# Kernel optimization log

Measured on AMD Instinct MI355X. Metric: run time of the kernel, lower is better.

The kernel has to match this reference:

```python
import jax, jax.numpy as jnp
import numpy as np
from jax import lax

NUM_HOP = 2      # opt.num_hop
POOL_HOP = 1     # Encoder(..., num_hop=1) in gnn_pools
K_POOL = 1024    # int(pooling_ratio * num_patches) = 0.5 * 2048
TH = 0.0         # opt.nonzero_th
T = 0.07         # NCE temperature
NEG_FILL = -10.0


def l2norm(x):
    # Normalize(power=2): x / (sum(x^2, dim=1, keepdim)^(1/2))
    return x / jnp.sqrt(jnp.sum(x * x, axis=1, keepdims=True))


def tagconv(A, h, W, b, k):
    # DGL TAGConv: concat_{i=0..k} (D^-1/2 A D^-1/2)^i h, then linear
    deg = jnp.sum(A, axis=1)
    dinv = lax.rsqrt(jnp.maximum(deg, 1e-12))
    An = A * dinv[:, None] * dinv[None, :]   # [N,N] normalized adjacency
    feats = [h]
    for _ in range(k):
        h = An @ h
        feats.append(h)
    return jnp.concatenate(feats, axis=1) @ W + b


def nce_pair(f_t, f_s):
    # calc_gnn NCE: positives = diag(f_t . f_s); negatives = full gram with diag masked to -10
    n = f_t.shape[0]
    eye = jnp.eye(n, dtype=bool)
    pos = jnp.sum(f_t * f_s, axis=1, keepdims=True)          # [N,1]
    neg_s = jnp.where(eye, NEG_FILL, f_t @ f_s.T)            # [N,N]
    neg_t = jnp.where(eye, NEG_FILL, f_s @ f_t.T)
    out_s = jnp.concatenate([pos, neg_s], axis=1) / T
    out_t = jnp.concatenate([pos, neg_t], axis=1) / T
    # CrossEntropy with label 0 == -log_softmax(out)[:, 0], mean over rows
    loss_s = -jnp.mean(jax.nn.log_softmax(out_s, axis=1)[:, 0])
    loss_t = -jnp.mean(jax.nn.log_softmax(out_t, axis=1)[:, 0])
    return loss_s + loss_t


def setup_inputs() -> dict:
    key = jax.random.key(0)
    ks = jax.random.split(key, 8)
    N, C, D = 2048, 512, 128
    g = 0.02  # init_gain ('normal' init)
    return {
        "fs": jax.random.normal(ks[0], (N, C), jnp.float32),
        "ft": jax.random.normal(ks[1], (N, C), jnp.float32),
        "W_embed": g * jax.random.normal(ks[2], (C, D), jnp.float32),
        "b_embed": jnp.zeros((D,), jnp.float32),
        "W_gnn": g * jax.random.normal(ks[3], ((NUM_HOP + 1) * D, D), jnp.float32),
        "b_gnn": jnp.zeros((D,), jnp.float32),
        "W_pool": g * jax.random.normal(ks[4], (D, 1), jnp.float32),
        "b_pool": jnp.zeros((1,), jnp.float32),
        "W_gnnp": g * jax.random.normal(ks[5], ((POOL_HOP + 1) * D, D), jnp.float32),
        "b_gnnp": jnp.zeros((D,), jnp.float32),
    }


def reference(fs, ft, W_embed, b_embed, W_gnn, b_gnn, W_pool, b_pool, W_gnnp, b_gnnp):
    # Embed: linear + l2 norm
    f_es = l2norm(fs @ W_embed + b_embed)   # student [N, nc]
    f_et = l2norm(ft @ W_embed + b_embed)   # teacher [N, nc]

    # nonzero_graph on detached teacher features; same adjacency reused for student
    ft_d = lax.stop_gradient(f_et)
    n = f_et.shape[0]
    eye = jnp.eye(n, dtype=bool)
    A = (ft_d @ ft_d.T > TH).astype(f_et.dtype)
    A = jnp.where(eye, 1.0, A)  # dgl.add_self_loop

    # TAGConv encoder + l2norm; teacher branch detached
    f_gt = lax.stop_gradient(l2norm(tagconv(A, f_et, W_gnn, b_gnn, NUM_HOP)))
    f_gs = l2norm(tagconv(A, f_es, W_gnn, b_gnn, NUM_HOP))
    loss_g = nce_pair(f_gt, f_gs)

    # Pool / top_k_graph
    scores = jax.nn.sigmoid((f_gt @ W_pool + b_pool)[:, 0])   # [N]
    vals, idx = lax.top_k(scores, K_POOL)
    new_ht = f_gt[idx] * vals[:, None]
    new_hs = f_gs[idx] * vals[:, None]
    un = (A > 0).astype(A.dtype)
    un2 = ((un @ un) > 0).astype(A.dtype)        # 2-hop boolean adjacency
    sub = un2[idx][:, idx]                       # [k,k]
    deg = jnp.sum(sub, axis=1)
    g_pool = sub / deg[None, :]                  # replicates torch broadcast in norm_g(g/degrees)

    # pooled-stage Encoder (TAGConv k=1) on the pooled graph structure (with self loops)
    k = K_POOL
    eye_k = jnp.eye(k, dtype=bool)
    Ap = (g_pool > 0).astype(A.dtype)
    Ap = jnp.where(eye_k, 1.0, Ap)
    f_pt = lax.stop_gradient(l2norm(tagconv(Ap, new_ht, W_gnnp, b_gnnp, POOL_HOP)))
    f_ps = l2norm(tagconv(Ap, new_hs, W_gnnp, b_gnnp, POOL_HOP))
    loss_pool = nce_pair(f_pt, f_ps)

    return loss_g + loss_pool
```

## Files before the change

kernel.cpp:

```cpp
#include <hip/hip_runtime.h>


#define TINV (1.0f / 0.07f)

using short8 = __attribute__((ext_vector_type(8))) short;
using f32x4  = __attribute__((ext_vector_type(4))) float;

__device__ __forceinline__ unsigned short f2bf(float f) {
    unsigned u = __float_as_uint(f);
    u += 0x7fff + ((u >> 16) & 1);
    return (unsigned short)(u >> 16);
}

template<bool BT>
__device__ __forceinline__ void mm_tile(const float* __restrict__ A, int lda,
                                        const float* __restrict__ B, int ldb,
                                        int i0, int j0, int k0, int k1,
                                        float (&acc)[4][4],
                                        float (&As)[16][68], float (&Bs)[16][68])
{
    const int tid = threadIdx.x;
    const int tx = tid & 15;
    const int ty = tid >> 4;
    const int lr = tid >> 2;
    const int lc = (tid & 3) * 4;
    for (int k = k0; k < k1; k += 16) {
        float4 av = *(const float4*)(A + (size_t)(i0 + lr) * lda + (k + lc));
        As[lc + 0][lr] = av.x; As[lc + 1][lr] = av.y;
        As[lc + 2][lr] = av.z; As[lc + 3][lr] = av.w;
        if (BT) {
            float4 bv = *(const float4*)(B + (size_t)(j0 + lr) * ldb + (k + lc));
            Bs[lc + 0][lr] = bv.x; Bs[lc + 1][lr] = bv.y;
            Bs[lc + 2][lr] = bv.z; Bs[lc + 3][lr] = bv.w;
        } else {
            const int n = tid & 63;
            const int kb = tid >> 6;
#pragma unroll
            for (int it = 0; it < 4; ++it)
                Bs[kb * 4 + it][n] = B[(size_t)(k + kb * 4 + it) * ldb + (j0 + n)];
        }
        __syncthreads();
#pragma unroll
        for (int kk = 0; kk < 16; ++kk) {
            float a[4], b[4];
#pragma unroll
            for (int u = 0; u < 4; ++u) a[u] = As[kk][ty * 4 + u];
#pragma unroll
            for (int v = 0; v < 4; ++v) b[v] = Bs[kk][tx * 4 + v];
#pragma unroll
            for (int u = 0; u < 4; ++u)
#pragma unroll
                for (int v = 0; v < 4; ++v)
                    acc[u][v] = fmaf(a[u], b[v], acc[u][v]);
        }
        __syncthreads();
    }
}

__launch_bounds__(256)
__global__ void k_setup_embed(const float* __restrict__ fs, const float* __restrict__ ft,
                              const float* __restrict__ W, float* __restrict__ part,
                              size_t zstr, int* __restrict__ zwords, int zcount,
                              float* __restrict__ out,
                              const float* __restrict__ Wg, const float* __restrict__ Wp,
                              unsigned short* __restrict__ Wtall)
{
    __shared__ float As[16][68];
    __shared__ float Bs[16][68];
    const int b = blockIdx.x;
    const int tid = threadIdx.x;
    if (b < 512) {
        const int z = b & 3;
        const int by = (b >> 2) & 63;
        const int bx = b >> 8;
        const float* A = (by < 32) ? ft : fs;
        const int i0 = (by & 31) * 64;
        const int j0 = bx * 64;
        float acc[4][4] = {};
        mm_tile<false>(A, 512, W, 128, i0, j0, z * 128, z * 128 + 128, acc, As, Bs);
        const int tx = tid & 15, ty = tid >> 4;
        float* dst = part + (size_t)z * zstr;
#pragma unroll
        for (int u = 0; u < 4; ++u) {
            const size_t ri = (size_t)(by * 64 + ty * 4 + u) * 128 + j0 + tx * 4;
            float4 vv;
            vv.x = acc[u][0]; vv.y = acc[u][1]; vv.z = acc[u][2]; vv.w = acc[u][3];
            *(float4*)(dst + ri) = vv;
        }
    } else if (b < 561) {
        const int i = (b - 512) * 256 + tid;
        if (i < zcount) zwords[i] = 0;
        if (b == 512 && tid == 0) out[0] = 0.0f;
    } else {
        const int e0 = (b - 561) * 2048 + tid;
#pragma unroll
        for (int it = 0; it < 8; ++it) {
            const int e = e0 + it * 256;
            const int c = e >> 14;
            const int rem = e & 16383;
            const int n = rem >> 7, k = rem & 127;
            const float* src = (c < 3) ? (Wg + (size_t)c * 16384)
                                       : (Wp + (size_t)(c - 3) * 16384);
            Wtall[e] = f2bf(src[(size_t)k * 128 + n]);
        }
    }
}

__launch_bounds__(256)
__global__ void k_gram_fused(const float* __restrict__ f_e,
                             unsigned short* __restrict__ A01,
                             unsigned long long* __restrict__ bits,
                             int* __restrict__ deg)
{
    __shared__ float As[16][68];
    __shared__ float Bs[16][68];
    __shared__ unsigned char nib[64][16];
    __shared__ unsigned char nibT[64][16];
    __shared__ unsigned long long chk[64];
    __shared__ unsigned long long chkT[64];
    const int b = blockIdx.x;
    int by = (int)((sqrtf(8.0f * b + 1.0f) - 1.0f) * 0.5f);
    while ((by + 1) * (by + 2) / 2 <= b) ++by;
    while (by * (by + 1) / 2 > b) --by;
    const int bx = b - by * (by + 1) / 2;
    const int i0 = by * 64, j0 = bx * 64;
    float acc[4][4] = {};
    mm_tile<true>(f_e, 128, f_e, 128, i0, j0, 0, 128, acc, As, Bs);
    const int tid = threadIdx.x;
    const int tx = tid & 15, ty = tid >> 4;
    unsigned pb = 0;
#pragma unroll
    for (int u = 0; u < 4; ++u)
#pragma unroll
        for (int v = 0; v < 4; ++v) {
            bool pred = (acc[u][v] > 0.0f) || (i0 + ty * 4 + u == j0 + tx * 4 + v);
            pb |= (unsigned)pred << (u * 4 + v);
        }
#pragma unroll
    for (int u = 0; u < 4; ++u) nib[ty * 4 + u][tx] = (pb >> (4 * u)) & 15;
#pragma unroll
    for (int v = 0; v < 4; ++v) {
        unsigned nt = 0;
#pragma unroll
        for (int u = 0; u < 4; ++u) nt |= ((pb >> (u * 4 + v)) & 1u) << u;
        nibT[tx * 4 + v][ty] = nt;
    }
    __syncthreads();
    if (tid < 64) {
        unsigned long long c = 0;
#pragma unroll
        for (int t = 0; t < 16; ++t) c |= (unsigned long long)nib[tid][t] << (4 * t);
        chk[tid] = c;
        bits[(size_t)(i0 + tid) * 32 + (j0 >> 6)] = c;
        atomicAdd(&deg[i0 + tid], __popcll(c));
    } else if (tid < 128 && bx != by) {
        const int r = tid - 64;
        unsigned long long c = 0;
#pragma unroll
        for (int t = 0; t < 16; ++t) c |= (unsigned long long)nibT[r][t] << (4 * t);
        chkT[r] = c;
        bits[(size_t)(j0 + r) * 32 + (i0 >> 6)] = c;
        atomicAdd(&deg[j0 + r], __popcll(c));
    }
    __syncthreads();
#pragma unroll
    for (int it = 0; it < 4; ++it) {
        const int row = it * 16 + (tid >> 4);
        const int c0 = (tid & 15) * 4;
        unsigned short o[4];
#pragma unroll
        for (int c = 0; c < 4; ++c)
            o[c] = ((chk[row] >> (c0 + c)) & 1) ? (unsigned short)0x3F80 : (unsigned short)0;
        *(ulonglong1*)&A01[(size_t)(i0 + row) * 2048 + j0 + c0] = *(ulonglong1*)o;
        if (bx != by) {
            unsigned short o2[4];
#pragma unroll
            for (int c = 0; c < 4; ++c)
                o2[c] = ((chkT[row] >> (c0 + c)) & 1) ? (unsigned short)0x3F80 : (unsigned short)0;
            *(ulonglong1*)&A01[(size_t)(j0 + row) * 2048 + i0 + c0] = *(ulonglong1*)o2;
        }
    }
}

__launch_bounds__(256)
__global__ void mm_bf16(const unsigned short* __restrict__ A, int lda, size_t aZ,
                        const unsigned short* __restrict__ B, int ldb, size_t bZ,
                        float* __restrict__ C, int ldc, size_t cZ,
                        int Kc, int kZ)
{
    __shared__ unsigned short As[64][40];
    __shared__ unsigned short Bs[128][40];
    const int tid = threadIdx.x;
    const int bz = blockIdx.z;
    const int i0 = blockIdx.y * 64;
    const int j0 = blockIdx.x * 128;
    const int k0 = bz * kZ;
    const unsigned short* Ab = A + (size_t)bz * aZ;
    const unsigned short* Bb = B + (size_t)bz * bZ;
    float* Cb = C + (size_t)bz * cZ;
    const int w = tid >> 6;
    const int lane = tid & 63;
    const int m = lane & 15;
    const int q = lane >> 4;
    f32x4 acc[8];
#pragma unroll
    for (int t = 0; t < 8; ++t)
#pragma unroll
        for (int r = 0; r < 4; ++r) acc[t][r] = 0.0f;

    const int ar = tid >> 2;
    const int ac = (tid & 3) * 8;
    for (int ks = 0; ks < Kc; ks += 32) {
        const int k = k0 + ks;
        *(ulonglong2*)&As[ar][ac] =
            *(const ulonglong2*)(Ab + (size_t)(i0 + ar) * lda + k + ac);
        *(ulonglong2*)&Bs[ar][ac] =
            *(const ulonglong2*)(Bb + (size_t)(j0 + ar) * ldb + k + ac);
        *(ulonglong2*)&Bs[ar + 64][ac] =
            *(const ulonglong2*)(Bb + (size_t)(j0 + ar + 64) * ldb + k + ac);
        __syncthreads();
        short8 a = *(const short8*)&As[w * 16 + m][q * 8];
#pragma unroll
        for (int nt = 0; nt < 8; ++nt) {
            short8 b = *(const short8*)&Bs[nt * 16 + m][q * 8];
            acc[nt] = __builtin_amdgcn_mfma_f32_16x16x32_bf16(a, b, acc[nt], 0, 0, 0);
        }
        __syncthreads();
    }
#pragma unroll
    for (int nt = 0; nt < 8; ++nt) {
        const int col = j0 + nt * 16 + m;
#pragma unroll
        for (int r = 0; r < 4; ++r) {
            const int row = i0 + w * 16 + q * 4 + r;
            Cb[(size_t)row * ldc + col] = acc[nt][r];
        }
    }
}

__global__ void reduce_hop(const float* __restrict__ part, int nz, size_t zstr,
                           int M, const float* __restrict__ dinv,
                           unsigned short* __restrict__ hb,
                           unsigned short* __restrict__ xt)
{
    __shared__ float T[32][33];
    const int tid = threadIdx.x;
    const int iloc = tid >> 3, nq = (tid & 7) * 4;
    const int n = blockIdx.x * 32 + nq;
    const int i = blockIdx.y * 32 + iloc;
    float4 s = *(const float4*)(part + (size_t)i * 256 + n);
    for (int z = 1; z < nz; ++z) {
        float4 t = *(const float4*)(part + (size_t)z * zstr + (size_t)i * 256 + n);
        s.x += t.x; s.y += t.y; s.z += t.z; s.w += t.w;
    }
    const float d = dinv[i];
    unsigned short o[4] = { f2bf(s.x * d), f2bf(s.y * d), f2bf(s.z * d), f2bf(s.w * d) };
    const int hrow = (n >= 128 ? M : 0) + i;
    *(ulonglong1*)(hb + (size_t)hrow * 128 + (n & 127)) = *(ulonglong1*)o;
    if (xt) {
        const float d2 = d * d;
        T[nq + 0][iloc] = s.x * d2; T[nq + 1][iloc] = s.y * d2;
        T[nq + 2][iloc] = s.z * d2; T[nq + 3][iloc] = s.w * d2;
        __syncthreads();
        const int nloc = tid >> 3, ic = (tid & 7) * 4;
        unsigned short o2[4];
#pragma unroll
        for (int c = 0; c < 4; ++c) o2[c] = f2bf(T[nloc][ic + c]);
        *(ulonglong1*)(xt + (size_t)(blockIdx.x * 32 + nloc) * M + blockIdx.y * 32 + ic) =
            *(ulonglong1*)o2;
    }
}

__global__ void combine_norm(const float* __restrict__ part, int nz, size_t zstr,
                             const float* __restrict__ bias,
                             float* __restrict__ f32out,
                             unsigned short* __restrict__ bf16out,
                             const float* __restrict__ Wp, const float* __restrict__ bp,
                             float* __restrict__ scores)
{
    const int row = blockIdx.x;
    const int tid = threadIdx.x;
    float v = bias[tid];
    for (int z = 0; z < nz; ++z) v += part[(size_t)z * zstr + (size_t)row * 128 + tid];
    __shared__ float red[128];
    red[tid] = v * v;
    __syncthreads();
    for (int s = 64; s > 0; s >>= 1) {
        if (tid < s) red[tid] += red[tid + s];
        __syncthreads();
    }
    const float o = v * (1.0f / sqrtf(red[0]));
    if (f32out)  f32out[(size_t)row * 128 + tid] = o;
    if (bf16out) bf16out[(size_t)row * 128 + tid] = f2bf(o);
    if (scores && row < 2048) {
        __syncthreads();
        red[tid] = o * Wp[tid];
        __syncthreads();
        for (int s = 64; s > 0; s >>= 1) {
            if (tid < s) red[tid] += red[tid + s];
            __syncthreads();
        }
        if (tid == 0) scores[row] = 1.0f / (1.0f + expf(-(red[0] + bp[0])));
    }
}

__global__ void make_xt(const float* __restrict__ f_e, const int* __restrict__ deg,
                        unsigned short* __restrict__ xt, float* __restrict__ dinv)
{
    __shared__ float T[32][33];
    const int b = blockIdx.x;
    const int bx = b & 7, by = b >> 3;
    const int tid = threadIdx.x;
    const int iloc = tid >> 3, nq = (tid & 7) * 4;
    const int n0 = bx * 32;
    const int i = by * 32 + iloc;
    const int srow = (n0 >= 128 ? 2048 : 0) + i;
    float4 f = *(const float4*)(f_e + (size_t)srow * 128 + ((n0 + nq) & 127));
    const float d = 1.0f / sqrtf((float)deg[i]);
    if (bx == 0 && (tid & 7) == 0) dinv[i] = d;
    T[nq + 0][iloc] = f.x * d; T[nq + 1][iloc] = f.y * d;
    T[nq + 2][iloc] = f.z * d; T[nq + 3][iloc] = f.w * d;
    __syncthreads();
    const int nloc = tid >> 3, ic = (tid & 7) * 4;
    unsigned short o[4];
#pragma unroll
    for (int c = 0; c < 4; ++c) o[c] = f2bf(T[nloc][ic + c]);
    *(ulonglong1*)(xt + (size_t)(n0 + nloc) * 2048 + by * 32 + ic) = *(ulonglong1*)o;
}

__launch_bounds__(256)
__global__ void k_nce_topk(const unsigned short* __restrict__ A,
                           const unsigned short* __restrict__ B,
                           float* __restrict__ rowsum, float* __restrict__ colsum,
                           float* __restrict__ pos, int gramBlocks, int bw,
                           const float* __restrict__ scores,
                           float* __restrict__ vals, int* __restrict__ idx)
{
    __shared__ unsigned short As[64][40];
    __shared__ unsigned short Bs[128][40];
    __shared__ float colbuf[4][128];
    __shared__ unsigned sv[2048];
    __shared__ int hist[256];
    __shared__ int shp, shr, sh_base, sh_out, wsum[5];
    const int tid = threadIdx.x;
    const int b = blockIdx.x;
    if (b < gramBlocks) {
        const int bx = b % bw, by = b / bw;
        const int i0 = by * 64;
        const int j0 = bx * 128;
        const int w = tid >> 6;
        const int lane = tid & 63;
        const int m = lane & 15;
        const int q = lane >> 4;
        f32x4 acc[8];
#pragma unroll
        for (int t = 0; t < 8; ++t)
#pragma unroll
            for (int r = 0; r < 4; ++r) acc[t][r] = 0.0f;
        const int ar = tid >> 2;
        const int ac = (tid & 3) * 8;
        for (int k = 0; k < 128; k += 32) {
            *(ulonglong2*)&As[ar][ac] =
                *(const ulonglong2*)(A + (size_t)(i0 + ar) * 128 + k + ac);
            *(ulonglong2*)&Bs[ar][ac] =
                *(const ulonglong2*)(B + (size_t)(j0 + ar) * 128 + k + ac);
            *(ulonglong2*)&Bs[ar + 64][ac] =
                *(const ulonglong2*)(B + (size_t)(j0 + ar + 64) * 128 + k + ac);
            __syncthreads();
            short8 a = *(const short8*)&As[w * 16 + m][q * 8];
#pragma unroll
            for (int nt = 0; nt < 8; ++nt) {
                short8 bb = *(const short8*)&Bs[nt * 16 + m][q * 8];
                acc[nt] = __builtin_amdgcn_mfma_f32_16x16x32_bf16(a, bb, acc[nt], 0, 0, 0);
            }
            __syncthreads();
        }
        float rpart[4] = {0.0f, 0.0f, 0.0f, 0.0f};
        float cpart[8];
#pragma unroll
        for (int nt = 0; nt < 8; ++nt) {
            const int col = j0 + nt * 16 + m;
            float cs = 0.0f;
#pragma unroll
            for (int r = 0; r < 4; ++r) {
                const int row = i0 + w * 16 + q * 4 + r;
                float g = acc[nt][r];
                float e = __expf(g * TINV);
                if (row == col) { pos[row] = g; e = 0.0f; }
                rpart[r] += e;
                cs += e;
            }
            cpart[nt] = cs;
        }
#pragma unroll
        for (int r = 0; r < 4; ++r) {
            float v = rpart[r];
            v += __shfl_xor(v, 1); v += __shfl_xor(v, 2);
            v += __shfl_xor(v, 4); v += __shfl_xor(v, 8);
            if (m == 0) atomicAdd(&rowsum[i0 + w * 16 + q * 4 + r], v);
        }
#pragma unroll
        for (int nt = 0; nt < 8; ++nt) {
            float v = cpart[nt];
            v += __shfl_xor(v, 16); v += __shfl_xor(v, 32);
            if (q == 0) colbuf[w][nt * 16 + m] = v;
        }
        __syncthreads();
        if (tid < 128) {
            float v = colbuf[0][tid] + colbuf[1][tid] + colbuf[2][tid] + colbuf[3][tid];
            atomicAdd(&colsum[j0 + tid], v);
        }
    } else {
        for (int e = tid; e < 2048; e += 256) sv[e] = __float_as_uint(scores[e]);
        if (tid == 0) { shp = 0; shr = 1024; sh_base = 0; sh_out = 0; }
        __syncthreads();
        for (int byte = 3; byte >= 0; --byte) {
            hist[tid] = 0;
            __syncthreads();
            const unsigned pref = (unsigned)shp;
            const unsigned pmask = (byte == 3) ? 0u : (0xFFFFFFFFu << ((byte + 1) * 8));
            for (int e = tid; e < 2048; e += 256) {
                unsigned u = sv[e];
                if ((u & pmask) == (pref & pmask))
                    atomicAdd(&hist[(u >> (byte * 8)) & 255], 1);
            }
            __syncthreads();
            if (tid == 0) {
                int rem = shr, bs = 255;
                for (; bs > 0; --bs) {
                    if (hist[bs] >= rem) break;
                    rem -= hist[bs];
                }
                shp = (int)(pref | ((unsigned)bs << (byte * 8)));
                shr = rem;
            }
            __syncthreads();
        }
        const unsigned t = (unsigned)shp;
        const int remain = shr;
        const int lane = tid & 63, wave = tid >> 6;
        for (int pass = 0; pass < 8; ++pass) {
            const int e = pass * 256 + tid;
            const unsigned u = sv[e];
            const bool eq = (u == t);
            unsigned long long mk = __ballot(eq);
            int wpre = __popcll(mk & ((1ull << lane) - 1ull));
            if (lane == 0) wsum[wave] = __popcll(mk);
            __syncthreads();
            if (tid == 0) {
                int a = sh_base;
                for (int ww = 0; ww < 4; ++ww) { int c = wsum[ww]; wsum[ww] = a; a += c; }
                sh_base = a;
            }
            __syncthreads();
            const int rank = eq ? (wsum[wave] + wpre) : 0x7fffffff;
            if ((u > t) || (eq && rank < remain)) {
                int slot = atomicAdd(&sh_out, 1);
                idx[slot] = e;
                vals[slot] = __uint_as_float(u);
            }
            __syncthreads();
        }
    }
}

__global__ void k_final_ap(const float* __restrict__ rs, const float* __restrict__ cs,
                           const float* __restrict__ pos, float* __restrict__ out,
                           const unsigned long long* __restrict__ bits,
                           const int* __restrict__ idx,
                           unsigned short* __restrict__ Ap, int* __restrict__ degp)
{
    __shared__ unsigned long long pb[32][33];
    __shared__ unsigned long long qb[32][33];
    __shared__ float red[256];
    const int b = blockIdx.x;
    const int tid = threadIdx.x;
    if (b < 1024) {
        const int tp = (b >> 5) * 32;
        const int tq = (b & 31) * 32;
        for (int t = tid; t < 1024; t += 256) {
            int r = t >> 5, w = t & 31;
            pb[r][w] = bits[(size_t)idx[tp + r] * 32 + w];
            qb[r][w] = bits[(size_t)idx[tq + r] * 32 + w];
        }
        __syncthreads();
        const int pi = tid >> 3;
        const int qc0 = (tid & 7) * 4;
        unsigned long long a0 = 0, a1 = 0, a2 = 0, a3 = 0;
#pragma unroll
        for (int w = 0; w < 32; ++w) {
            const unsigned long long p = pb[pi][w];
            a0 |= p & qb[qc0 + 0][w];
            a1 |= p & qb[qc0 + 1][w];
            a2 |= p & qb[qc0 + 2][w];
            a3 |= p & qb[qc0 + 3][w];
        }
        unsigned short o[4] = { (unsigned short)(a0 ? 0x3F80 : 0),
                                (unsigned short)(a1 ? 0x3F80 : 0),
                                (unsigned short)(a2 ? 0x3F80 : 0),
                                (unsigned short)(a3 ? 0x3F80 : 0) };
        *(ulonglong1*)&Ap[(size_t)(tp + pi) * 1024 + tq + qc0] = *(ulonglong1*)o;
        int v = (a0 ? 1 : 0) + (a1 ? 1 : 0) + (a2 ? 1 : 0) + (a3 ? 1 : 0);
        v += __shfl_xor(v, 1); v += __shfl_xor(v, 2); v += __shfl_xor(v, 4);
        if ((tid & 7) == 0) atomicAdd(&degp[tp + pi], v);
    } else {
        const int i = (b - 1024) * 256 + tid;
        float p = pos[i] * TINV;
        float ep = __expf(p);
        float t = (logf(rs[i] + ep) - p) + (logf(cs[i] + ep) - p);
        red[tid] = t;
        __syncthreads();
        for (int s = 128; s > 0; s >>= 1) {
            if (tid < s) red[tid] += red[tid + s];
            __syncthreads();
        }
        if (tid == 0) atomicAdd(out, red[0] * (1.0f / 2048.0f));
    }
}

__global__ void nce_final(const float* __restrict__ rs, const float* __restrict__ cs,
                          const float* __restrict__ pos, float invN,
                          float* __restrict__ out)
{
    const int i = blockIdx.x * 256 + threadIdx.x;
    float p = pos[i] * TINV;
    float ep = __expf(p);
    float t = (logf(rs[i] + ep) - p) + (logf(cs[i] + ep) - p);
    __shared__ float red[256];
    red[threadIdx.x] = t;
    __syncthreads();
    for (int s = 128; s > 0; s >>= 1) {
        if (threadIdx.x < s) red[threadIdx.x] += red[threadIdx.x + s];
        __syncthreads();
    }
    if (threadIdx.x == 0) atomicAdd(out, red[0] * invN);
}

__global__ void gather_xt(const float* __restrict__ f_g, const int* __restrict__ idx,
                          const float* __restrict__ vals, const int* __restrict__ degp,
                          unsigned short* __restrict__ new_hb,
                          unsigned short* __restrict__ xtp, float* __restrict__ dinvp)
{
    __shared__ float T[32][33];
    const int b = blockIdx.x;
    const int bx = b & 7, by = b >> 3;
    const int tid = threadIdx.x;
    const int ploc = tid >> 3, nq = (tid & 7) * 4;
    const int n0 = bx * 32;
    const int p = by * 32 + ploc;
    const int s = idx[p];
    const float v = vals[p];
    const float dp = 1.0f / sqrtf((float)degp[p]);
    if (bx == 0 && (tid & 7) == 0) dinvp[p] = dp;
    const int srow = (n0 >= 128 ? 2048 : 0) + s;
    float4 f = *(const float4*)(f_g + (size_t)srow * 128 + ((n0 + nq) & 127));
    f.x *= v; f.y *= v; f.z *= v; f.w *= v;
    unsigned short o[4] = { f2bf(f.x), f2bf(f.y), f2bf(f.z), f2bf(f.w) };
    const int hrow = (n0 >= 128 ? 1024 : 0) + p;
    *(ulonglong1*)(new_hb + (size_t)hrow * 128 + ((n0 + nq) & 127)) = *(ulonglong1*)o;
    T[nq + 0][ploc] = f.x * dp; T[nq + 1][ploc] = f.y * dp;
    T[nq + 2][ploc] = f.z * dp; T[nq + 3][ploc] = f.w * dp;
    __syncthreads();
    const int nloc = tid >> 3, pc = (tid & 7) * 4;
    unsigned short o2[4];
#pragma unroll
    for (int c = 0; c < 4; ++c) o2[c] = f2bf(T[nloc][pc + c]);
    *(ulonglong1*)(xtp + (size_t)(n0 + nloc) * 1024 + by * 32 + pc) = *(ulonglong1*)o2;
}

extern "C" void kernel_launch(void* const* d_in, const int* in_sizes, int n_in,
                              void* d_out, int out_size, void* d_ws, size_t ws_size,
                              hipStream_t stream)
{
    (void)in_sizes; (void)n_in; (void)out_size; (void)ws_size;
    const float* fs      = (const float*)d_in[0];
    const float* ft      = (const float*)d_in[1];
    const float* W_embed = (const float*)d_in[2];
    const float* b_embed = (const float*)d_in[3];
    const float* W_gnn   = (const float*)d_in[4];
    const float* b_gnn   = (const float*)d_in[5];
    const float* W_pool  = (const float*)d_in[6];
    const float* b_pool  = (const float*)d_in[7];
    const float* W_gnnp  = (const float*)d_in[8];
    const float* b_gnnp  = (const float*)d_in[9];
    float* out = (float*)d_out;

    float* ws = (float*)d_ws;
    size_t o = 0;
    auto alloc = [&](size_t n) { float* p = ws + o; o += (n + 3) & ~3ull; return p; };
    float* bigB   = alloc(2048ull * 2048);
    float* f_e    = alloc(4096 * 128);
    float* f_g    = alloc(4096 * 128);
    unsigned short* A01  = (unsigned short*)alloc(2048ull * 2048 / 2);
    unsigned short* febT = (unsigned short*)alloc(3ull * 4096 * 128 / 2);
    unsigned short* Xt1  = (unsigned short*)alloc(256ull * 2048 / 2);
    unsigned short* Xt2  = (unsigned short*)alloc(256ull * 2048 / 2);
    unsigned short* f_gb = (unsigned short*)alloc(4096ull * 128 / 2);
    unsigned short* Wtall= (unsigned short*)alloc(5ull * 16384 / 2);
    unsigned short* Ap01 = (unsigned short*)alloc(1024ull * 1024 / 2);
    unsigned short* nhb  = (unsigned short*)alloc(2ull * 2048 * 128 / 2);
    unsigned short* Xtp  = (unsigned short*)alloc(256ull * 1024 / 2);
    unsigned short* f_pb = (unsigned short*)alloc(2048ull * 128 / 2);
    float* dinv   = alloc(2048);
    float* scores = alloc(2048);
    float* vals   = alloc(1024);
    int*   idxb   = (int*)alloc(1024);
    float* dinvp  = alloc(1024);
    unsigned long long* bits = (unsigned long long*)alloc(2048 * 32 * 2);
    float* nceb = alloc(9216);
    int*   deg  = (int*)alloc(2048);
    int*   degp = (int*)alloc(1024);
    const int kZeroCount = 9216 + 2048 + 1024;

    const size_t FSTR = 4096ull * 128;
    const size_t PSTR = 1024ull * 256;
    unsigned short* feb = febT;
    unsigned short* h1b = febT + FSTR;
    unsigned short* h2b = febT + 2 * FSTR;
    unsigned short* tmpb = nhb + 2048ull * 128;
    unsigned short* Wt  = Wtall;
    unsigned short* WtP = Wtall + 3ull * 16384;
    float* rs  = nceb;
    float* csu = nceb + 2048;
    float* pos = nceb + 4096;
    float* rsp  = nceb + 6144;
    float* csp  = nceb + 7168;
    float* posp = nceb + 8192;

    k_setup_embed<<<601, 256, 0, stream>>>(fs, ft, W_embed, bigB, FSTR,
                                           (int*)nceb, kZeroCount, out, W_gnn, W_gnnp, Wtall);
    combine_norm<<<4096, 128, 0, stream>>>(bigB, 4, FSTR, b_embed, f_e, feb,
                                           nullptr, nullptr, nullptr);
    k_gram_fused<<<528, 256, 0, stream>>>(f_e, A01, bits, deg);
    make_xt<<<512, 256, 0, stream>>>(f_e, deg, Xt1, dinv);
    mm_bf16<<<dim3(2, 32, 4), 256, 0, stream>>>(A01, 2048, 0, Xt1, 2048, 0,
                                                bigB, 256, FSTR, 512, 512);
    reduce_hop<<<dim3(8, 64), 256, 0, stream>>>(bigB, 4, FSTR, 2048, dinv, h1b, Xt2);
    mm_bf16<<<dim3(2, 32, 4), 256, 0, stream>>>(A01, 2048, 0, Xt2, 2048, 0,
                                                bigB, 256, FSTR, 512, 512);
    reduce_hop<<<dim3(8, 64), 256, 0, stream>>>(bigB, 4, FSTR, 2048, dinv, h2b, nullptr);
    mm_bf16<<<dim3(1, 64, 3), 256, 0, stream>>>(feb, 128, FSTR, Wt, 128, 16384,
                                                bigB, 128, FSTR, 128, 0);
    combine_norm<<<4096, 128, 0, stream>>>(bigB, 3, FSTR, b_gnn, f_g, f_gb,
                                           W_pool, b_pool, scores);
    k_nce_topk<<<513, 256, 0, stream>>>(f_gb, f_gb + 2048 * 128, rs, csu, pos,
                                        512, 16, scores, vals, idxb);
    k_final_ap<<<1032, 256, 0, stream>>>(rs, csu, pos, out, bits, idxb, Ap01, degp);
    gather_xt<<<256, 256, 0, stream>>>(f_g, idxb, vals, degp, nhb, Xtp, dinvp);
    mm_bf16<<<dim3(2, 16, 4), 256, 0, stream>>>(Ap01, 1024, 0, Xtp, 1024, 0,
                                                bigB, 256, PSTR, 256, 256);
    reduce_hop<<<dim3(8, 32), 256, 0, stream>>>(bigB, 4, PSTR, 1024, dinvp, tmpb, nullptr);
    mm_bf16<<<dim3(1, 32, 2), 256, 0, stream>>>(nhb, 128, 2048ull * 128, WtP, 128, 16384,
                                                bigB, 128, PSTR, 128, 0);
    combine_norm<<<2048, 128, 0, stream>>>(bigB, 2, PSTR, b_gnnp, nullptr, f_pb,
                                           nullptr, nullptr, nullptr);
    k_nce_topk<<<128, 256, 0, stream>>>(f_pb, f_pb + 1024 * 128, rsp, csp, posp,
                                        128, 8, nullptr, nullptr, nullptr);
    nce_final<<<4, 256, 0, stream>>>(rsp, csp, posp, 1.0f / 1024.0f, out);
}
```

Baseline: 214.8 us.

## Apply TAGConv weights before propagation via Horner form and fuse linear into gram kernel

```diff
diff --git a/kernel.cpp b/kernel.cpp
--- a/kernel.cpp
+++ b/kernel.cpp
@@ -57,6 +57,39 @@
     }
 }
 
+__device__ __forceinline__ void mm64x128(const unsigned short* __restrict__ Ab, int lda,
+                                         const unsigned short* __restrict__ Bb, int ldb,
+                                         int i0, int j0, int k0, int Kc,
+                                         f32x4 (&acc)[8],
+                                         unsigned short (&As)[64][40],
+                                         unsigned short (&Bs)[128][40])
+{
+    const int tid = threadIdx.x;
+    const int w = tid >> 6;
+    const int lane = tid & 63;
+    const int m = lane & 15;
+    const int q = lane >> 4;
+    const int ar = tid >> 2;
+    const int ac = (tid & 3) * 8;
+    for (int ks = 0; ks < Kc; ks += 32) {
+        const int k = k0 + ks;
+        *(ulonglong2*)&As[ar][ac] =
+            *(const ulonglong2*)(Ab + (size_t)(i0 + ar) * lda + k + ac);
+        *(ulonglong2*)&Bs[ar][ac] =
+            *(const ulonglong2*)(Bb + (size_t)(j0 + ar) * ldb + k + ac);
+        *(ulonglong2*)&Bs[ar + 64][ac] =
+            *(const ulonglong2*)(Bb + (size_t)(j0 + ar + 64) * ldb + k + ac);
+        __syncthreads();
+        short8 a = *(const short8*)&As[w * 16 + m][q * 8];
+#pragma unroll
+        for (int nt = 0; nt < 8; ++nt) {
+            short8 b = *(const short8*)&Bs[nt * 16 + m][q * 8];
+            acc[nt] = __builtin_amdgcn_mfma_f32_16x16x32_bf16(a, b, acc[nt], 0, 0, 0);
+        }
+        __syncthreads();
+    }
+}
+
 __launch_bounds__(256)
 __global__ void k_setup_embed(const float* __restrict__ fs, const float* __restrict__ ft,
                               const float* __restrict__ W, float* __restrict__ part,
@@ -106,19 +139,70 @@
     }
 }
 
+__global__ void combine_norm(const float* __restrict__ part, int nz, size_t zstr,
+                             const float* __restrict__ bias,
+                             float* __restrict__ f32out,
+                             unsigned short* __restrict__ bf16out)
+{
+    const int row = blockIdx.x;
+    const int tid = threadIdx.x;
+    float v = bias[tid];
+    for (int z = 0; z < nz; ++z) v += part[(size_t)z * zstr + (size_t)row * 128 + tid];
+    __shared__ float red[128];
+    red[tid] = v * v;
+    __syncthreads();
+    for (int s = 64; s > 0; s >>= 1) {
+        if (tid < s) red[tid] += red[tid + s];
+        __syncthreads();
+    }
+    const float o = v * (1.0f / sqrtf(red[0]));
+    f32out[(size_t)row * 128 + tid] = o;
+    bf16out[(size_t)row * 128 + tid] = f2bf(o);
+}
+
 __launch_bounds__(256)
 __global__ void k_gram_fused(const float* __restrict__ f_e,
                              unsigned short* __restrict__ A01,
                              unsigned long long* __restrict__ bits,
-                             int* __restrict__ deg)
-{
-    __shared__ float As[16][68];
-    __shared__ float Bs[16][68];
-    __shared__ unsigned char nib[64][16];
-    __shared__ unsigned char nibT[64][16];
-    __shared__ unsigned long long chk[64];
-    __shared__ unsigned long long chkT[64];
+                             int* __restrict__ deg,
+                             const unsigned short* __restrict__ feb,
+                             const unsigned short* __restrict__ Wt,
+                             float* __restrict__ hW)
+{
+    __shared__ __align__(16) unsigned char smem[15360];
     const int b = blockIdx.x;
+    const int tid = threadIdx.x;
+    if (b >= 528) {
+        unsigned short (&As2)[64][40]  = *reinterpret_cast<unsigned short(*)[64][40]>(smem);
+        unsigned short (&Bs2)[128][40] = *reinterpret_cast<unsigned short(*)[128][40]>(smem + 5120);
+        const int lb = b - 528;
+        const int z = lb >> 6;
+        const int i0 = (lb & 63) * 64;
+        f32x4 acc[8];
+#pragma unroll
+        for (int t = 0; t < 8; ++t)
+#pragma unroll
+            for (int r = 0; r < 4; ++r) acc[t][r] = 0.0f;
+        mm64x128(feb, 128, Wt + (size_t)z * 16384, 128, i0, 0, 0, 128, acc, As2, Bs2);
+        const int w = tid >> 6, lane = tid & 63, m = lane & 15, q = lane >> 4;
+        float* Cb = hW + (size_t)z * (4096ull * 128);
+#pragma unroll
+        for (int nt = 0; nt < 8; ++nt) {
+            const int col = nt * 16 + m;
+#pragma unroll
+            for (int r = 0; r < 4; ++r) {
+                const int row = i0 + w * 16 + q * 4 + r;
+                Cb[(size_t)row * 128 + col] = acc[nt][r];
+            }
+        }
+        return;
+    }
+    float (&As)[16][68] = *reinterpret_cast<float(*)[16][68]>(smem);
+    float (&Bs)[16][68] = *reinterpret_cast<float(*)[16][68]>(smem + 4352);
+    unsigned char (&nib)[64][16]  = *reinterpret_cast<unsigned char(*)[64][16]>(smem + 8704);
+    unsigned char (&nibT)[64][16] = *reinterpret_cast<unsigned char(*)[64][16]>(smem + 9728);
+    unsigned long long (&chk)[64]  = *reinterpret_cast<unsigned long long(*)[64]>(smem + 10752);
+    unsigned long long (&chkT)[64] = *reinterpret_cast<unsigned long long(*)[64]>(smem + 11264);
     int by = (int)((sqrtf(8.0f * b + 1.0f) - 1.0f) * 0.5f);
     while ((by + 1) * (by + 2) / 2 <= b) ++by;
     while (by * (by + 1) / 2 > b) --by;
@@ -126,7 +210,6 @@
     const int i0 = by * 64, j0 = bx * 64;
     float acc[4][4] = {};
     mm_tile<true>(f_e, 128, f_e, 128, i0, j0, 0, 128, acc, As, Bs);
-    const int tid = threadIdx.x;
     const int tx = tid & 15, ty = tid >> 4;
     unsigned pb = 0;
 #pragma unroll
@@ -198,35 +281,13 @@
     const unsigned short* Ab = A + (size_t)bz * aZ;
     const unsigned short* Bb = B + (size_t)bz * bZ;
     float* Cb = C + (size_t)bz * cZ;
-    const int w = tid >> 6;
-    const int lane = tid & 63;
-    const int m = lane & 15;
-    const int q = lane >> 4;
     f32x4 acc[8];
 #pragma unroll
     for (int t = 0; t < 8; ++t)
 #pragma unroll
         for (int r = 0; r < 4; ++r) acc[t][r] = 0.0f;
-
-    const int ar = tid >> 2;
-    const int ac = (tid & 3) * 8;
-    for (int ks = 0; ks < Kc; ks += 32) {
-        const int k = k0 + ks;
-        *(ulonglong2*)&As[ar][ac] =
-            *(const ulonglong2*)(Ab + (size_t)(i0 + ar) * lda + k + ac);
-        *(ulonglong2*)&Bs[ar][ac] =
-            *(const ulonglong2*)(Bb + (size_t)(j0 + ar) * ldb + k + ac);
-        *(ulonglong2*)&Bs[ar + 64][ac] =
-            *(const ulonglong2*)(Bb + (size_t)(j0 + ar + 64) * ldb + k + ac);
-        __syncthreads();
-        short8 a = *(const short8*)&As[w * 16 + m][q * 8];
-#pragma unroll
-        for (int nt = 0; nt < 8; ++nt) {
-            short8 b = *(const short8*)&Bs[nt * 16 + m][q * 8];
-            acc[nt] = __builtin_amdgcn_mfma_f32_16x16x32_bf16(a, b, acc[nt], 0, 0, 0);
-        }
-        __syncthreads();
-    }
+    mm64x128(Ab, lda, Bb, ldb, i0, j0, k0, Kc, acc, As, Bs);
+    const int w = tid >> 6, lane = tid & 63, m = lane & 15, q = lane >> 4;
 #pragma unroll
     for (int nt = 0; nt < 8; ++nt) {
         const int col = j0 + nt * 16 + m;
@@ -238,10 +299,10 @@
     }
 }
 
-__global__ void reduce_hop(const float* __restrict__ part, int nz, size_t zstr,
-                           int M, const float* __restrict__ dinv,
-                           unsigned short* __restrict__ hb,
-                           unsigned short* __restrict__ xt)
+__global__ void reduce_xt(const float* __restrict__ part, int nz, size_t zstr,
+                          int M, const float* __restrict__ dinv,
+                          const float* __restrict__ addT,
+                          unsigned short* __restrict__ xt)
 {
     __shared__ float T[32][33];
     const int tid = threadIdx.x;
@@ -254,57 +315,62 @@
         s.x += t.x; s.y += t.y; s.z += t.z; s.w += t.w;
     }
     const float d = dinv[i];
-    unsigned short o[4] = { f2bf(s.x * d), f2bf(s.y * d), f2bf(s.z * d), f2bf(s.w * d) };
-    const int hrow = (n >= 128 ? M : 0) + i;
-    *(ulonglong1*)(hb + (size_t)hrow * 128 + (n & 127)) = *(ulonglong1*)o;
-    if (xt) {
-        const float d2 = d * d;
-        T[nq + 0][iloc] = s.x * d2; T[nq + 1][iloc] = s.y * d2;
-        T[nq + 2][iloc] = s.z * d2; T[nq + 3][iloc] = s.w * d2;
-        __syncthreads();
-        const int nloc = tid >> 3, ic = (tid & 7) * 4;
-        unsigned short o2[4];
-#pragma unroll
-        for (int c = 0; c < 4; ++c) o2[c] = f2bf(T[nloc][ic + c]);
-        *(ulonglong1*)(xt + (size_t)(blockIdx.x * 32 + nloc) * M + blockIdx.y * 32 + ic) =
-            *(ulonglong1*)o2;
-    }
-}
-
-__global__ void combine_norm(const float* __restrict__ part, int nz, size_t zstr,
-                             const float* __restrict__ bias,
-                             float* __restrict__ f32out,
-                             unsigned short* __restrict__ bf16out,
-                             const float* __restrict__ Wp, const float* __restrict__ bp,
-                             float* __restrict__ scores)
+    const int srow = (n >= 128 ? M : 0) + i;
+    float4 a = *(const float4*)(addT + (size_t)srow * 128 + (n & 127));
+    T[nq + 0][iloc] = (a.x + s.x * d) * d;
+    T[nq + 1][iloc] = (a.y + s.y * d) * d;
+    T[nq + 2][iloc] = (a.z + s.z * d) * d;
+    T[nq + 3][iloc] = (a.w + s.w * d) * d;
+    __syncthreads();
+    const int nloc = tid >> 3, ic = (tid & 7) * 4;
+    unsigned short o2[4];
+#pragma unroll
+    for (int c = 0; c < 4; ++c) o2[c] = f2bf(T[nloc][ic + c]);
+    *(ulonglong1*)(xt + (size_t)(blockIdx.x * 32 + nloc) * M + blockIdx.y * 32 + ic) =
+        *(ulonglong1*)o2;
+}
+
+__global__ void combine_tag(const float* __restrict__ part, int nz, size_t zstr,
+                            int Mnodes,
+                            const float* __restrict__ add,
+                            const float* __restrict__ dinv,
+                            const float* __restrict__ bias,
+                            float* __restrict__ f32out,
+                            unsigned short* __restrict__ bf16out,
+                            const float* __restrict__ Wp, const float* __restrict__ bp,
+                            float* __restrict__ scores)
 {
     const int row = blockIdx.x;
     const int tid = threadIdx.x;
-    float v = bias[tid];
-    for (int z = 0; z < nz; ++z) v += part[(size_t)z * zstr + (size_t)row * 128 + tid];
+    const int node = (row < Mnodes) ? row : row - Mnodes;
+    const int boff = (row < Mnodes) ? 0 : 128;
+    float s = 0.0f;
+    for (int z = 0; z < nz; ++z)
+        s += part[(size_t)z * zstr + (size_t)node * 256 + boff + tid];
+    float v = bias[tid] + add[(size_t)row * 128 + tid] + dinv[node] * s;
     __shared__ float red[128];
     red[tid] = v * v;
     __syncthreads();
-    for (int s = 64; s > 0; s >>= 1) {
-        if (tid < s) red[tid] += red[tid + s];
+    for (int st = 64; st > 0; st >>= 1) {
+        if (tid < st) red[tid] += red[tid + st];
         __syncthreads();
     }
     const float o = v * (1.0f / sqrtf(red[0]));
-    if (f32out)  f32out[(size_t)row * 128 + tid] = o;
-    if (bf16out) bf16out[(size_t)row * 128 + tid] = f2bf(o);
-    if (scores && row < 2048) {
+    if (f32out) f32out[(size_t)row * 128 + tid] = o;
+    bf16out[(size_t)row * 128 + tid] = f2bf(o);
+    if (Wp && row < Mnodes) {
         __syncthreads();
         red[tid] = o * Wp[tid];
         __syncthreads();
-        for (int s = 64; s > 0; s >>= 1) {
-            if (tid < s) red[tid] += red[tid + s];
+        for (int st = 64; st > 0; st >>= 1) {
+            if (tid < st) red[tid] += red[tid + st];
             __syncthreads();
         }
         if (tid == 0) scores[row] = 1.0f / (1.0f + expf(-(red[0] + bp[0])));
     }
 }
 
-__global__ void make_xt(const float* __restrict__ f_e, const int* __restrict__ deg,
+__global__ void make_xt(const float* __restrict__ src, const int* __restrict__ deg,
                         unsigned short* __restrict__ xt, float* __restrict__ dinv)
 {
     __shared__ float T[32][33];
@@ -315,7 +381,7 @@
     const int n0 = bx * 32;
     const int i = by * 32 + iloc;
     const int srow = (n0 >= 128 ? 2048 : 0) + i;
-    float4 f = *(const float4*)(f_e + (size_t)srow * 128 + ((n0 + nq) & 127));
+    float4 f = *(const float4*)(src + (size_t)srow * 128 + ((n0 + nq) & 127));
     const float d = 1.0f / sqrtf((float)deg[i]);
     if (bx == 0 && (tid & 7) == 0) dinv[i] = d;
     T[nq + 0][iloc] = f.x * d; T[nq + 1][iloc] = f.y * d;
@@ -357,24 +423,7 @@
         for (int t = 0; t < 8; ++t)
 #pragma unroll
             for (int r = 0; r < 4; ++r) acc[t][r] = 0.0f;
-        const int ar = tid >> 2;
-        const int ac = (tid & 3) * 8;
-        for (int k = 0; k < 128; k += 32) {
-            *(ulonglong2*)&As[ar][ac] =
-                *(const ulonglong2*)(A + (size_t)(i0 + ar) * 128 + k + ac);
-            *(ulonglong2*)&Bs[ar][ac] =
-                *(const ulonglong2*)(B + (size_t)(j0 + ar) * 128 + k + ac);
-            *(ulonglong2*)&Bs[ar + 64][ac] =
-                *(const ulonglong2*)(B + (size_t)(j0 + ar + 64) * 128 + k + ac);
-            __syncthreads();
-            short8 a = *(const short8*)&As[w * 16 + m][q * 8];
-#pragma unroll
-            for (int nt = 0; nt < 8; ++nt) {
-                short8 bb = *(const short8*)&Bs[nt * 16 + m][q * 8];
-                acc[nt] = __builtin_amdgcn_mfma_f32_16x16x32_bf16(a, bb, acc[nt], 0, 0, 0);
-            }
-            __syncthreads();
-        }
+        mm64x128(A, 128, B, 128, i0, j0, 0, 128, acc, As, Bs);
         float rpart[4] = {0.0f, 0.0f, 0.0f, 0.0f};
         float cpart[8];
 #pragma unroll
@@ -536,36 +585,71 @@
     if (threadIdx.x == 0) atomicAdd(out, red[0] * invN);
 }
 
-__global__ void gather_xt(const float* __restrict__ f_g, const int* __restrict__ idx,
+__global__ void gather_nh(const float* __restrict__ f_g, const int* __restrict__ idx,
                           const float* __restrict__ vals, const int* __restrict__ degp,
-                          unsigned short* __restrict__ new_hb,
-                          unsigned short* __restrict__ xtp, float* __restrict__ dinvp)
-{
-    __shared__ float T[32][33];
+                          unsigned short* __restrict__ nhb, float* __restrict__ dinvp)
+{
     const int b = blockIdx.x;
-    const int bx = b & 7, by = b >> 3;
-    const int tid = threadIdx.x;
-    const int ploc = tid >> 3, nq = (tid & 7) * 4;
-    const int n0 = bx * 32;
-    const int p = by * 32 + ploc;
+    const int tid = threadIdx.x;
+    if (b < 4) {
+        const int p2 = b * 256 + tid;
+        dinvp[p2] = 1.0f / sqrtf((float)degp[p2]);
+    }
+    const int hrow = b * 8 + (tid >> 5);
+    const int cq = (tid & 31) * 4;
+    const int p = hrow & 1023;
     const int s = idx[p];
     const float v = vals[p];
-    const float dp = 1.0f / sqrtf((float)degp[p]);
-    if (bx == 0 && (tid & 7) == 0) dinvp[p] = dp;
-    const int srow = (n0 >= 128 ? 2048 : 0) + s;
-    float4 f = *(const float4*)(f_g + (size_t)srow * 128 + ((n0 + nq) & 127));
-    f.x *= v; f.y *= v; f.z *= v; f.w *= v;
-    unsigned short o[4] = { f2bf(f.x), f2bf(f.y), f2bf(f.z), f2bf(f.w) };
-    const int hrow = (n0 >= 128 ? 1024 : 0) + p;
-    *(ulonglong1*)(new_hb + (size_t)hrow * 128 + ((n0 + nq) & 127)) = *(ulonglong1*)o;
-    T[nq + 0][ploc] = f.x * dp; T[nq + 1][ploc] = f.y * dp;
-    T[nq + 2][ploc] = f.z * dp; T[nq + 3][ploc] = f.w * dp;
-    __syncthreads();
-    const int nloc = tid >> 3, pc = (tid & 7) * 4;
-    unsigned short o2[4];
-#pragma unroll
-    for (int c = 0; c < 4; ++c) o2[c] = f2bf(T[nloc][pc + c]);
-    *(ulonglong1*)(xtp + (size_t)(n0 + nloc) * 1024 + by * 32 + pc) = *(ulonglong1*)o2;
+    const int srow = (hrow >= 1024 ? 2048 : 0) + s;
+    float4 f = *(const float4*)(f_g + (size_t)srow * 128 + cq);
+    unsigned short o[4] = { f2bf(f.x * v), f2bf(f.y * v), f2bf(f.z * v), f2bf(f.w * v) };
+    *(ulonglong1*)&nhb[(size_t)hrow * 128 + cq] = *(ulonglong1*)o;
+}
+
+__launch_bounds__(256)
+__global__ void k_lin_pool(const unsigned short* __restrict__ nhb,
+                           const unsigned short* __restrict__ WtP,
+                           const float* __restrict__ dinvp,
+                           float* __restrict__ P0,
+                           unsigned short* __restrict__ Xtp)
+{
+    __shared__ unsigned short As[64][40];
+    __shared__ unsigned short Bs[128][40];
+    const int b = blockIdx.x;
+    const int z = b >> 5;
+    const int i0 = (b & 31) * 64;
+    const int tid = threadIdx.x;
+    f32x4 acc[8];
+#pragma unroll
+    for (int t = 0; t < 8; ++t)
+#pragma unroll
+        for (int r = 0; r < 4; ++r) acc[t][r] = 0.0f;
+    mm64x128(nhb, 128, WtP + (size_t)z * 16384, 128, i0, 0, 0, 128, acc, As, Bs);
+    const int w = tid >> 6, lane = tid & 63, m = lane & 15, q = lane >> 4;
+    if (z == 0) {
+#pragma unroll
+        for (int nt = 0; nt < 8; ++nt) {
+            const int col = nt * 16 + m;
+#pragma unroll
+            for (int r = 0; r < 4; ++r) {
+                const int row = i0 + w * 16 + q * 4 + r;
+                P0[(size_t)row * 128 + col] = acc[nt][r];
+            }
+        }
+    } else {
+        const int boff = (i0 >= 1024) ? 128 : 0;
+        const int p0 = (i0 & 1023) + w * 16 + q * 4;
+        float4 dv = *(const float4*)(dinvp + p0);
+        const float dvr[4] = { dv.x, dv.y, dv.z, dv.w };
+#pragma unroll
+        for (int nt = 0; nt < 8; ++nt) {
+            const int n = boff + nt * 16 + m;
+            unsigned short o[4];
+#pragma unroll
+            for (int r = 0; r < 4; ++r) o[r] = f2bf(acc[nt][r] * dvr[r]);
+            *(ulonglong1*)&Xtp[(size_t)n * 1024 + p0] = *(ulonglong1*)o;
+        }
+    }
 }
 
 extern "C" void kernel_launch(void* const* d_in, const int* in_sizes, int n_in,
@@ -592,15 +676,17 @@
     float* f_e    = alloc(4096 * 128);
     float* f_g    = alloc(4096 * 128);
     unsigned short* A01  = (unsigned short*)alloc(2048ull * 2048 / 2);
-    unsigned short* febT = (unsigned short*)alloc(3ull * 4096 * 128 / 2);
+    unsigned short* feb  = (unsigned short*)alloc(4096ull * 128 / 2);
     unsigned short* Xt1  = (unsigned short*)alloc(256ull * 2048 / 2);
     unsigned short* Xt2  = (unsigned short*)alloc(256ull * 2048 / 2);
     unsigned short* f_gb = (unsigned short*)alloc(4096ull * 128 / 2);
     unsigned short* Wtall= (unsigned short*)alloc(5ull * 16384 / 2);
     unsigned short* Ap01 = (unsigned short*)alloc(1024ull * 1024 / 2);
-    unsigned short* nhb  = (unsigned short*)alloc(2ull * 2048 * 128 / 2);
+    unsigned short* nhb  = (unsigned short*)alloc(2048ull * 128 / 2);
     unsigned short* Xtp  = (unsigned short*)alloc(256ull * 1024 / 2);
     unsigned short* f_pb = (unsigned short*)alloc(2048ull * 128 / 2);
+    float* hW     = alloc(3ull * 4096 * 128);
+    float* P0     = alloc(2048ull * 128);
     float* dinv   = alloc(2048);
     float* scores = alloc(2048);
     float* vals   = alloc(1024);
@@ -614,12 +700,11 @@
 
     const size_t FSTR = 4096ull * 128;
     const size_t PSTR = 1024ull * 256;
-    unsigned short* feb = febT;
-    unsigned short* h1b = febT + FSTR;
-    unsigned short* h2b = febT + 2 * FSTR;
-    unsigned short* tmpb = nhb + 2048ull * 128;
     unsigned short* Wt  = Wtall;
     unsigned short* WtP = Wtall + 3ull * 16384;
+    float* hW0 = hW;
+    float* hW1 = hW + FSTR;
+    float* hW2 = hW + 2 * FSTR;
     float* rs  = nceb;
     float* csu = nceb + 2048;
     float* pos = nceb + 4096;
@@ -629,31 +714,25 @@
 
     k_setup_embed<<<601, 256, 0, stream>>>(fs, ft, W_embed, bigB, FSTR,
                                            (int*)nceb, kZeroCount, out, W_gnn, W_gnnp, Wtall);
-    combine_norm<<<4096, 128, 0, stream>>>(bigB, 4, FSTR, b_embed, f_e, feb,
-                                           nullptr, nullptr, nullptr);
-    k_gram_fused<<<528, 256, 0, stream>>>(f_e, A01, bits, deg);
-    make_xt<<<512, 256, 0, stream>>>(f_e, deg, Xt1, dinv);
+    combine_norm<<<4096, 128, 0, stream>>>(bigB, 4, FSTR, b_embed, f_e, feb);
+    k_gram_fused<<<720, 256, 0, stream>>>(f_e, A01, bits, deg, feb, Wt, hW);
+    make_xt<<<512, 256, 0, stream>>>(hW2, deg, Xt1, dinv);
     mm_bf16<<<dim3(2, 32, 4), 256, 0, stream>>>(A01, 2048, 0, Xt1, 2048, 0,
                                                 bigB, 256, FSTR, 512, 512);
-    reduce_hop<<<dim3(8, 64), 256, 0, stream>>>(bigB, 4, FSTR, 2048, dinv, h1b, Xt2);
+    reduce_xt<<<dim3(8, 64), 256, 0, stream>>>(bigB, 4, FSTR, 2048, dinv, hW1, Xt2);
     mm_bf16<<<dim3(2, 32, 4), 256, 0, stream>>>(A01, 2048, 0, Xt2, 2048, 0,
                                                 bigB, 256, FSTR, 512, 512);
-    reduce_hop<<<dim3(8, 64), 256, 0, stream>>>(bigB, 4, FSTR, 2048, dinv, h2b, nullptr);
-    mm_bf16<<<dim3(1, 64, 3), 256, 0, stream>>>(feb, 128, FSTR, Wt, 128, 16384,
-                                                bigB, 128, FSTR, 128, 0);
-    combine_norm<<<4096, 128, 0, stream>>>(bigB, 3, FSTR, b_gnn, f_g, f_gb,
-                                           W_pool, b_pool, scores);
+    combine_tag<<<4096, 128, 0, stream>>>(bigB, 4, FSTR, 2048, hW0, dinv, b_gnn,
+                                          f_g, f_gb, W_pool, b_pool, scores);
     k_nce_topk<<<513, 256, 0, stream>>>(f_gb, f_gb + 2048 * 128, rs, csu, pos,
                                         512, 16, scores, vals, idxb);
     k_final_ap<<<1032, 256, 0, stream>>>(rs, csu, pos, out, bits, idxb, Ap01, degp);
-    gather_xt<<<256, 256, 0, stream>>>(f_g, idxb, vals, degp, nhb, Xtp, dinvp);
+    gather_nh<<<256, 256, 0, stream>>>(f_g, idxb, vals, degp, nhb, dinvp);
+    k_lin_pool<<<64, 256, 0, stream>>>(nhb, WtP, dinvp, P0, Xtp);
     mm_bf16<<<dim3(2, 16, 4), 256, 0, stream>>>(Ap01, 1024, 0, Xtp, 1024, 0,
                                                 bigB, 256, PSTR, 256, 256);
-    reduce_hop<<<dim3(8, 32), 256, 0, stream>>>(bigB, 4, PSTR, 1024, dinvp, tmpb, nullptr);
-    mm_bf16<<<dim3(1, 32, 2), 256, 0, stream>>>(nhb, 128, 2048ull * 128, WtP, 128, 16384,
-                                                bigB, 128, PSTR, 128, 0);
-    combine_norm<<<2048, 128, 0, stream>>>(bigB, 2, PSTR, b_gnnp, nullptr, f_pb,
-                                           nullptr, nullptr, nullptr);
+    combine_tag<<<2048, 128, 0, stream>>>(bigB, 4, PSTR, 1024, P0, dinvp, b_gnnp,
+                                          nullptr, f_pb, nullptr, nullptr, nullptr);
     k_nce_topk<<<128, 256, 0, stream>>>(f_pb, f_pb + 1024 * 128, rsp, csp, posp,
                                         128, 8, nullptr, nullptr, nullptr);
     nce_final<<<4, 256, 0, stream>>>(rsp, csp, posp, 1.0f / 1024.0f, out);
```

New measurement: 208.3 us. 3.0% less time.
